# Performance work log

Measured on AMD Instinct MI355X. Metric: run time of the kernel, lower is better.

Reference implementation:

```python
import jax, jax.numpy as jnp
import numpy as np

N_NODES = 100000
N_EDGES = 1600000
IN_CH, HID, OUT_CH = 512, 128, 64
K_HOPS = 2
LN_EPS = 1e-5


def _layernorm(h, gamma, beta):
    mu = jnp.mean(h, axis=-1, keepdims=True)
    var = jnp.var(h, axis=-1, keepdims=True)
    return (h - mu) * jax.lax.rsqrt(var + LN_EPS) * gamma + beta


def setup_inputs() -> dict:
    key = jax.random.key(0)
    ks = jax.random.split(key, 12)
    x = jax.random.normal(ks[0], (N_NODES, IN_CH), dtype=jnp.float32)
    edge_index = jax.random.randint(ks[1], (2, N_EDGES), 0, N_NODES, dtype=jnp.int64)
    s1 = 1.0 / np.sqrt(IN_CH)
    s2 = 1.0 / np.sqrt(HID)
    return {
        "x": x,
        "edge_index": edge_index,
        "W1": jax.random.normal(ks[2], (IN_CH, HID), dtype=jnp.float32) * s1,
        "b1": jnp.zeros((HID,), dtype=jnp.float32),
        "g1": jnp.ones((HID,), dtype=jnp.float32),
        "be1": jnp.zeros((HID,), dtype=jnp.float32),
        "Wc": jax.random.normal(ks[3], (HID, HID), dtype=jnp.float32) * s2,
        "bc": jnp.zeros((HID,), dtype=jnp.float32),
        "g2": jnp.ones((HID,), dtype=jnp.float32),
        "be2": jnp.zeros((HID,), dtype=jnp.float32),
        "W2": jax.random.normal(ks[4], (HID, OUT_CH), dtype=jnp.float32) * s2,
        "b2": jnp.zeros((OUT_CH,), dtype=jnp.float32),
    }


def reference(x, edge_index, W1, b1, g1, be1, Wc, bc, g2, be2, W2, b2):
    N = x.shape[0]
    # lin1 -> GELU(exact) -> LayerNorm (dropout is identity in eval)
    h = jax.nn.gelu(x @ W1 + b1, approximate=False)
    h = _layernorm(h, g1, be1)

    # SGConv: add self-loops, symmetric normalization, K-hop propagation, then Linear
    loop = jnp.arange(N, dtype=edge_index.dtype)
    src = jnp.concatenate([edge_index[0], loop])
    dst = jnp.concatenate([edge_index[1], loop])
    w = jnp.ones(src.shape[0], dtype=h.dtype)
    deg = jax.ops.segment_sum(w, dst, num_segments=N)
    dinv = jnp.where(deg > 0, jax.lax.rsqrt(deg), 0.0)
    norm = (dinv[src] * dinv[dst])[:, None]  # [E+N, 1]
    for _ in range(K_HOPS):
        h = jax.ops.segment_sum(h[src] * norm, dst, num_segments=N)
    h = h @ Wc + bc

    h = jax.nn.gelu(h, approximate=False)
    h = _layernorm(h, g2, be2)
    return h @ W2 + b2
```

## Files before the change

kernel.cpp:

```cpp
#include <hip/hip_runtime.h>
#include <math.h>

#define N_NODES 100000
#define N_EDGES 1600000
#define IN_CH 512
#define HID 128
#define OUT_CH 64
#define NBUCK ((N_NODES + 255) / 256)
#define LBUF_CAP 8192

typedef __attribute__((ext_vector_type(8))) short bf16x8;
typedef __attribute__((ext_vector_type(4))) float f32x4;

__device__ __forceinline__ float gelu_exact(float v) {
    return 0.5f * v * (1.0f + erff(v * 0.70710678118654752440f));
}

__device__ __forceinline__ unsigned short bf16r(float f) {
    union { float f; unsigned int u; } v;
    v.f = f;
    unsigned int r = v.u + 0x7fffu + ((v.u >> 16) & 1u);
    return (unsigned short)(r >> 16);
}

__device__ __forceinline__ float bf16f(unsigned short h) {
    union { unsigned int u; float f; } v;
    v.u = ((unsigned int)h) << 16;
    return v.f;
}

__global__ void bzero(int* __restrict__ bcnt) {
    if (threadIdx.x < NBUCK) bcnt[threadIdx.x] = 0;
}

__global__ __launch_bounds__(256) void bhist(const int* __restrict__ dst,
                                             int* __restrict__ bcnt, int e) {
    __shared__ int lcnt[NBUCK];
    for (int i = threadIdx.x; i < NBUCK; i += 256) lcnt[i] = 0;
    __syncthreads();
    int base = blockIdx.x * 256 * 16 + threadIdx.x;
#pragma unroll
    for (int i = 0; i < 16; i++) {
        int id = base + i * 256;
        if (id < e) atomicAdd(&lcnt[dst[id] >> 8], 1);
    }
    __syncthreads();
    for (int i = threadIdx.x; i < NBUCK; i += 256)
        if (lcnt[i]) atomicAdd(&bcnt[i], lcnt[i]);
}

__global__ void bscan(const int* __restrict__ bcnt, int* __restrict__ bbase,
                      int* __restrict__ bcur, int* __restrict__ rowptr, int e) {
    __shared__ int tmp[512];
    int i = threadIdx.x;
    int v = (i < NBUCK) ? bcnt[i] : 0;
    tmp[i] = v;
    __syncthreads();
#pragma unroll
    for (int o = 1; o < 512; o <<= 1) {
        int t = (i >= o) ? tmp[i - o] : 0;
        __syncthreads();
        tmp[i] += t;
        __syncthreads();
    }
    if (i <= NBUCK) {
        int excl = (i == 0) ? 0 : tmp[i - 1];
        bbase[i] = excl;
        if (i < NBUCK) bcur[i] = excl;
    }
    if (i == 0) rowptr[N_NODES] = e;
}

__global__ __launch_bounds__(256) void binA(const int* __restrict__ src,
                                            const int* __restrict__ dst,
                                            int* __restrict__ bcur,
                                            unsigned int* __restrict__ ebuf, int e) {
    __shared__ int lcnt[NBUCK];
    __shared__ int gbase[NBUCK];
    const int tid = threadIdx.x;
    for (int i = tid; i < NBUCK; i += 256) lcnt[i] = 0;
    __syncthreads();
    const int base = blockIdx.x * (256 * 16);
    int sv[16];
    short bk[16], rk[16];
    unsigned char ld[16];
#pragma unroll
    for (int i = 0; i < 16; i++) {
        int idx = base + tid + i * 256;
        bk[i] = -1;
        if (idx < e) {
            int d = dst[idx];
            sv[i] = src[idx];
            ld[i] = (unsigned char)(d & 255);
            int b = d >> 8;
            bk[i] = (short)b;
            rk[i] = (short)atomicAdd(&lcnt[b], 1);
        }
    }
    __syncthreads();
    for (int i = tid; i < NBUCK; i += 256)
        if (lcnt[i]) gbase[i] = atomicAdd(&bcur[i], lcnt[i]);
    __syncthreads();
#pragma unroll
    for (int i = 0; i < 16; i++)
        if (bk[i] >= 0)
            ebuf[gbase[bk[i]] + rk[i]] = ((unsigned int)sv[i] << 8) | ld[i];
}

__global__ __launch_bounds__(256) void binB(const unsigned int* __restrict__ ebuf,
                                            const int* __restrict__ bbase,
                                            int* __restrict__ rowptr, int* __restrict__ eadj,
                                            float* __restrict__ dinv) {
    __shared__ int cnt[256], lofs[256], lcur[256];
    __shared__ int lbuf[LBUF_CAP];
    const int b = blockIdx.x, tid = threadIdx.x;
    const int n0 = b * 256;
    const int nn = min(256, N_NODES - n0);
    const int e0 = bbase[b], e1 = bbase[b + 1];
    const int ecount = e1 - e0;
    cnt[tid] = 0;
    __syncthreads();
    for (int i = tid; i < ecount; i += 256) atomicAdd(&cnt[ebuf[e0 + i] & 255], 1);
    __syncthreads();
    int v = cnt[tid];
    lofs[tid] = v;
    __syncthreads();
#pragma unroll
    for (int o = 1; o < 256; o <<= 1) {
        int t = (tid >= o) ? lofs[tid - o] : 0;
        __syncthreads();
        lofs[tid] += t;
        __syncthreads();
    }
    int excl = lofs[tid] - v;
    lcur[tid] = excl;
    if (tid < nn) {
        rowptr[n0 + tid] = e0 + excl;
        dinv[n0 + tid] = rsqrtf((float)(v + 1));
    }
    __syncthreads();
    for (int i = tid; i < ecount; i += 256) {
        unsigned int w = ebuf[e0 + i];
        int pos = atomicAdd(&lcur[w & 255], 1);
        int s = (int)(w >> 8);
        if (pos < LBUF_CAP) lbuf[pos] = s;
        else eadj[e0 + pos] = s;
    }
    __syncthreads();
    int lim = min(ecount, LBUF_CAP);
    for (int i = tid; i < lim; i += 256) eadj[e0 + i] = lbuf[i];
}

__global__ void conv_t(const float* __restrict__ in, unsigned short* __restrict__ out,
                       int Kdim, int Nc) {
    int idx = blockIdx.x * 256 + threadIdx.x;
    if (idx >= Kdim * Nc) return;
    int n = idx / Kdim, k = idx % Kdim;
    out[idx] = bf16r(in[(size_t)k * Nc + n]);
}

template <int K, int NT, bool A32, bool LN>
__global__ __launch_bounds__(256) void gemm_mfma(
    const void* __restrict__ Aptr, const unsigned short* __restrict__ BT,
    const float* __restrict__ bias, const float* __restrict__ gamma,
    const float* __restrict__ beta, void* __restrict__ Cptr, int M) {
    constexpr int BM = 64, N = NT * 16, NSTEP = K / 32;
    __shared__ unsigned short As[2][BM * 32];
    __shared__ unsigned short Bs[2][N * 32];
    const int tid = threadIdx.x;
    const int wave = tid >> 6, lane = tid & 63;
    const int l15 = lane & 15, quad = lane >> 4;
    const int row0 = blockIdx.x * BM;

    const int sr = tid >> 2, sc = tid & 3;
    const int sswz = sc ^ ((sr >> 2) & 3);
    const bool aok = (row0 + sr) < M;

    const float* A32p = (const float*)Aptr + (size_t)(row0 + sr) * K + sc * 8;
    const unsigned short* A16p = (const unsigned short*)Aptr + (size_t)(row0 + sr) * K + sc * 8;
    const unsigned short* B0p = BT + (size_t)sr * K + sc * 8;
    const unsigned short* B1p = BT + (size_t)(sr + 64) * K + sc * 8;

    float4 pa0, pa1;
    int4 pa16, pb0, pb1;
    if (A32) {
        pa0 = aok ? *(const float4*)(A32p) : make_float4(0.f, 0.f, 0.f, 0.f);
        pa1 = aok ? *(const float4*)(A32p + 4) : make_float4(0.f, 0.f, 0.f, 0.f);
    } else {
        pa16 = aok ? *(const int4*)(A16p) : make_int4(0, 0, 0, 0);
    }
    pb0 = *(const int4*)(B0p);
    if (NT == 8) pb1 = *(const int4*)(B1p);

    f32x4 acc[NT];
#pragma unroll
    for (int ni = 0; ni < NT; ni++) acc[ni] = (f32x4){0.f, 0.f, 0.f, 0.f};

    float bia[NT], gam[NT], bet[NT];
#pragma unroll
    for (int ni = 0; ni < NT; ni++) {
        bia[ni] = bias[ni * 16 + l15];
        if (LN) {
            gam[ni] = gamma[ni * 16 + l15];
            bet[ni] = beta[ni * 16 + l15];
        }
    }

    const int fswz = quad ^ ((l15 >> 2) & 3);
    const int aoff = (wave * 16 + l15) * 32 + fswz * 8;

    for (int step = 0; step < NSTEP; step++) {
        const int buf = step & 1;
        if (A32) {
            int4 w;
            w.x = (int)((unsigned int)bf16r(pa0.x) | ((unsigned int)bf16r(pa0.y) << 16));
            w.y = (int)((unsigned int)bf16r(pa0.z) | ((unsigned int)bf16r(pa0.w) << 16));
            w.z = (int)((unsigned int)bf16r(pa1.x) | ((unsigned int)bf16r(pa1.y) << 16));
            w.w = (int)((unsigned int)bf16r(pa1.z) | ((unsigned int)bf16r(pa1.w) << 16));
            *(int4*)&As[buf][sr * 32 + sswz * 8] = w;
        } else {
            *(int4*)&As[buf][sr * 32 + sswz * 8] = pa16;
        }
        *(int4*)&Bs[buf][sr * 32 + sswz * 8] = pb0;
        if (NT == 8) *(int4*)&Bs[buf][(sr + 64) * 32 + sswz * 8] = pb1;
        __syncthreads();
        if (step + 1 < NSTEP) {
            const int ko = (step + 1) * 32;
            if (A32) {
                pa0 = aok ? *(const float4*)(A32p + ko) : make_float4(0.f, 0.f, 0.f, 0.f);
                pa1 = aok ? *(const float4*)(A32p + ko + 4) : make_float4(0.f, 0.f, 0.f, 0.f);
            } else {
                pa16 = aok ? *(const int4*)(A16p + ko) : make_int4(0, 0, 0, 0);
            }
            pb0 = *(const int4*)(B0p + ko);
            if (NT == 8) pb1 = *(const int4*)(B1p + ko);
        }
        bf16x8 a = *(const bf16x8*)&As[buf][aoff];
#pragma unroll
        for (int ni = 0; ni < NT; ni++) {
            bf16x8 b = *(const bf16x8*)&Bs[buf][(ni * 16 + l15) * 32 + fswz * 8];
            acc[ni] = __builtin_amdgcn_mfma_f32_16x16x32_bf16(a, b, acc[ni], 0, 0, 0);
        }
    }

#pragma unroll
    for (int r = 0; r < 4; r++) {
        int grow = row0 + wave * 16 + quad * 4 + r;
        if (LN) {
            float g[NT];
            float s = 0.f, sq = 0.f;
#pragma unroll
            for (int ni = 0; ni < NT; ni++) {
                float v = gelu_exact(acc[ni][r] + bia[ni]);
                g[ni] = v;
                s += v;
                sq += v * v;
            }
#pragma unroll
            for (int m = 1; m < 16; m <<= 1) {
                s += __shfl_xor(s, m);
                sq += __shfl_xor(sq, m);
            }
            float mu = s * (1.0f / N);
            float var = sq * (1.0f / N) - mu * mu;
            float rs = rsqrtf(var + 1e-5f);
            if (grow < M) {
                unsigned short* C = (unsigned short*)Cptr;
#pragma unroll
                for (int ni = 0; ni < NT; ni++) {
                    float o = (g[ni] - mu) * rs * gam[ni] + bet[ni];
                    C[(size_t)grow * N + ni * 16 + l15] = bf16r(o);
                }
            }
        } else {
            if (grow < M) {
                float* C = (float*)Cptr;
#pragma unroll
                for (int ni = 0; ni < NT; ni++)
                    C[(size_t)grow * N + ni * 16 + l15] = acc[ni][r] + bia[ni];
            }
        }
    }
}

__global__ __launch_bounds__(256) void sgc_gather_bf16(const unsigned short* __restrict__ hin,
                                                       unsigned short* __restrict__ hout,
                                                       const int* __restrict__ rowptr,
                                                       const int* __restrict__ eadj,
                                                       const float* __restrict__ dinv, int n) {
    int row = blockIdx.x * 4 + (threadIdx.x >> 6);
    int lane = threadIdx.x & 63;
    if (row >= n) return;
    float di = dinv[row];
    unsigned int u = *(const unsigned int*)(hin + (size_t)row * HID + lane * 2);
    float ax = bf16f((unsigned short)(u & 0xffff)) * di * di;
    float ay = bf16f((unsigned short)(u >> 16)) * di * di;
    int j = rowptr[row], end = rowptr[row + 1];
    for (; j + 7 < end; j += 8) {
        int s[8];
        float dv[8];
        unsigned int uu[8];
#pragma unroll
        for (int t = 0; t < 8; t++) s[t] = eadj[j + t];
#pragma unroll
        for (int t = 0; t < 8; t++) dv[t] = dinv[s[t]];
#pragma unroll
        for (int t = 0; t < 8; t++)
            uu[t] = *(const unsigned int*)(hin + (size_t)s[t] * HID + lane * 2);
#pragma unroll
        for (int t = 0; t < 8; t++) {
            float w = di * dv[t];
            ax += bf16f((unsigned short)(uu[t] & 0xffff)) * w;
            ay += bf16f((unsigned short)(uu[t] >> 16)) * w;
        }
    }
    for (; j + 1 < end; j += 2) {
        int s0 = eadj[j], s1 = eadj[j + 1];
        float w0 = di * dinv[s0], w1 = di * dinv[s1];
        unsigned int u0 = *(const unsigned int*)(hin + (size_t)s0 * HID + lane * 2);
        unsigned int u1 = *(const unsigned int*)(hin + (size_t)s1 * HID + lane * 2);
        ax += bf16f((unsigned short)(u0 & 0xffff)) * w0 + bf16f((unsigned short)(u1 & 0xffff)) * w1;
        ay += bf16f((unsigned short)(u0 >> 16)) * w0 + bf16f((unsigned short)(u1 >> 16)) * w1;
    }
    if (j < end) {
        int s0 = eadj[j];
        float w = di * dinv[s0];
        unsigned int u0 = *(const unsigned int*)(hin + (size_t)s0 * HID + lane * 2);
        ax += bf16f((unsigned short)(u0 & 0xffff)) * w;
        ay += bf16f((unsigned short)(u0 >> 16)) * w;
    }
    unsigned int o = (unsigned int)bf16r(ax) | ((unsigned int)bf16r(ay) << 16);
    *(unsigned int*)(hout + (size_t)row * HID + lane * 2) = o;
}

extern "C" void kernel_launch(void* const* d_in, const int* in_sizes, int n_in,
                              void* d_out, int out_size, void* d_ws, size_t ws_size,
                              hipStream_t stream) {
    const float* x   = (const float*)d_in[0];
    const int*   ei  = (const int*)d_in[1];
    const float* W1  = (const float*)d_in[2];
    const float* b1  = (const float*)d_in[3];
    const float* g1  = (const float*)d_in[4];
    const float* be1 = (const float*)d_in[5];
    const float* Wc  = (const float*)d_in[6];
    const float* bc  = (const float*)d_in[7];
    const float* g2  = (const float*)d_in[8];
    const float* be2 = (const float*)d_in[9];
    const float* W2  = (const float*)d_in[10];
    const float* b2  = (const float*)d_in[11];
    float* out = (float*)d_out;

    const int N = in_sizes[0] / IN_CH;
    const int E = in_sizes[1] / 2;
    const int* src = ei;
    const int* dst = ei + E;

    char* ws = (char*)d_ws;
    size_t off = 0;
    auto alloc = [&](size_t bytes) {
        void* p = ws + off;
        off = (off + bytes + 255) & ~(size_t)255;
        return p;
    };
    float* dinv   = (float*)alloc((size_t)N * 4);
    int*   rowptr = (int*)alloc((size_t)(N + 1) * 4);
    int*   bcnt   = (int*)alloc((size_t)(NBUCK + 1) * 4);
    int*   bbase  = (int*)alloc((size_t)(NBUCK + 1) * 4);
    int*   bcur   = (int*)alloc((size_t)(NBUCK + 1) * 4);
    unsigned int* ebuf = (unsigned int*)alloc((size_t)E * 4);
    int*   eadj   = (int*)alloc((size_t)E * 4);
    unsigned short* W1T = (unsigned short*)alloc((size_t)HID * IN_CH * 2);
    unsigned short* WcT = (unsigned short*)alloc((size_t)HID * HID * 2);
    unsigned short* W2T = (unsigned short*)alloc((size_t)OUT_CH * HID * 2);
    unsigned short* hA  = (unsigned short*)alloc((size_t)N * HID * 2);
    unsigned short* hB  = (unsigned short*)alloc((size_t)N * HID * 2);

    const int B = 256;
    const int eblk16 = (E + 4095) / 4096;

    bzero<<<1, 512, 0, stream>>>(bcnt);
    bhist<<<eblk16, B, 0, stream>>>(dst, bcnt, E);
    bscan<<<1, 512, 0, stream>>>(bcnt, bbase, bcur, rowptr, E);
    binA<<<eblk16, B, 0, stream>>>(src, dst, bcur, ebuf, E);
    binB<<<NBUCK, B, 0, stream>>>(ebuf, bbase, rowptr, eadj, dinv);

    conv_t<<<(IN_CH * HID + 255) / 256, B, 0, stream>>>(W1, W1T, IN_CH, HID);
    conv_t<<<(HID * HID + 255) / 256, B, 0, stream>>>(Wc, WcT, HID, HID);
    conv_t<<<(HID * OUT_CH + 255) / 256, B, 0, stream>>>(W2, W2T, HID, OUT_CH);

    const int gblk = (N + 63) / 64;
    gemm_mfma<IN_CH, 8, true, true><<<gblk, B, 0, stream>>>(x, W1T, b1, g1, be1, hA, N);
    sgc_gather_bf16<<<(N + 3) / 4, B, 0, stream>>>(hA, hB, rowptr, eadj, dinv, N);
    sgc_gather_bf16<<<(N + 3) / 4, B, 0, stream>>>(hB, hA, rowptr, eadj, dinv, N);
    gemm_mfma<HID, 8, false, true><<<gblk, B, 0, stream>>>(hA, WcT, bc, g2, be2, hB, N);
    gemm_mfma<HID, 4, false, false><<<gblk, B, 0, stream>>>(hB, W2T, b2, nullptr, nullptr, out, N);
}
```

Baseline: 539.4 us.

## Fold symmetric normalization into node pre/post scaling and simplify gather

After: 530.2 us. About the same (-1.7%).

```diff
diff --git a/kernel.cpp b/kernel.cpp
--- a/kernel.cpp
+++ b/kernel.cpp
@@ -151,19 +151,37 @@
     for (int i = tid; i < lim; i += 256) eadj[e0 + i] = lbuf[i];
 }
 
-__global__ void conv_t(const float* __restrict__ in, unsigned short* __restrict__ out,
-                       int Kdim, int Nc) {
+__global__ __launch_bounds__(256) void conv_all(const float* __restrict__ W1,
+                                                const float* __restrict__ Wc,
+                                                const float* __restrict__ W2,
+                                                unsigned short* __restrict__ W1T,
+                                                unsigned short* __restrict__ WcT,
+                                                unsigned short* __restrict__ W2T) {
     int idx = blockIdx.x * 256 + threadIdx.x;
-    if (idx >= Kdim * Nc) return;
-    int n = idx / Kdim, k = idx % Kdim;
-    out[idx] = bf16r(in[(size_t)k * Nc + n]);
-}
-
-template <int K, int NT, bool A32, bool LN>
+    if (idx < IN_CH * HID) {
+        int n = idx / IN_CH, k = idx % IN_CH;
+        W1T[idx] = bf16r(W1[(size_t)k * HID + n]);
+        return;
+    }
+    idx -= IN_CH * HID;
+    if (idx < HID * HID) {
+        int n = idx / HID, k = idx % HID;
+        WcT[idx] = bf16r(Wc[(size_t)k * HID + n]);
+        return;
+    }
+    idx -= HID * HID;
+    if (idx < HID * OUT_CH) {
+        int n = idx / HID, k = idx % HID;
+        W2T[idx] = bf16r(W2[(size_t)k * OUT_CH + n]);
+    }
+}
+
+template <int K, int NT, bool A32, bool LN, bool SCALE>
 __global__ __launch_bounds__(256) void gemm_mfma(
     const void* __restrict__ Aptr, const unsigned short* __restrict__ BT,
     const float* __restrict__ bias, const float* __restrict__ gamma,
-    const float* __restrict__ beta, void* __restrict__ Cptr, int M) {
+    const float* __restrict__ beta, const float* __restrict__ dinvp,
+    void* __restrict__ Cptr, int M) {
     constexpr int BM = 64, N = NT * 16, NSTEP = K / 32;
     __shared__ unsigned short As[2][BM * 32];
     __shared__ unsigned short Bs[2][N * 32];
@@ -265,10 +283,13 @@
             float var = sq * (1.0f / N) - mu * mu;
             float rs = rsqrtf(var + 1e-5f);
             if (grow < M) {
+                float dv = 1.0f;
+                if (SCALE) dv = dinvp[grow];
                 unsigned short* C = (unsigned short*)Cptr;
 #pragma unroll
                 for (int ni = 0; ni < NT; ni++) {
                     float o = (g[ni] - mu) * rs * gam[ni] + bet[ni];
+                    if (SCALE) o *= dv;
                     C[(size_t)grow * N + ni * 16 + l15] = bf16r(o);
                 }
             }
@@ -287,48 +308,40 @@
                                                        unsigned short* __restrict__ hout,
                                                        const int* __restrict__ rowptr,
                                                        const int* __restrict__ eadj,
-                                                       const float* __restrict__ dinv, int n) {
-    int row = blockIdx.x * 4 + (threadIdx.x >> 6);
-    int lane = threadIdx.x & 63;
+                                                       const float* __restrict__ dinv,
+                                                       int n, int pw) {
+    int row = __builtin_amdgcn_readfirstlane(blockIdx.x * 4 + (threadIdx.x >> 6));
     if (row >= n) return;
-    float di = dinv[row];
-    unsigned int u = *(const unsigned int*)(hin + (size_t)row * HID + lane * 2);
-    float ax = bf16f((unsigned short)(u & 0xffff)) * di * di;
-    float ay = bf16f((unsigned short)(u >> 16)) * di * di;
-    int j = rowptr[row], end = rowptr[row + 1];
+    const int lane = threadIdx.x & 63;
+    const unsigned int* __restrict__ rows = (const unsigned int*)hin;
+    unsigned int u = rows[(size_t)row * 64 + lane];
+    float ax = bf16f((unsigned short)(u & 0xffff));
+    float ay = bf16f((unsigned short)(u >> 16));
+    int j = rowptr[row];
+    const int end = rowptr[row + 1];
     for (; j + 7 < end; j += 8) {
         int s[8];
-        float dv[8];
+#pragma unroll
+        for (int t = 0; t < 8; t++) s[t] = __builtin_amdgcn_readfirstlane(eadj[j + t]);
         unsigned int uu[8];
 #pragma unroll
-        for (int t = 0; t < 8; t++) s[t] = eadj[j + t];
-#pragma unroll
-        for (int t = 0; t < 8; t++) dv[t] = dinv[s[t]];
-#pragma unroll
-        for (int t = 0; t < 8; t++)
-            uu[t] = *(const unsigned int*)(hin + (size_t)s[t] * HID + lane * 2);
+        for (int t = 0; t < 8; t++) uu[t] = rows[(size_t)s[t] * 64 + lane];
 #pragma unroll
         for (int t = 0; t < 8; t++) {
-            float w = di * dv[t];
-            ax += bf16f((unsigned short)(uu[t] & 0xffff)) * w;
-            ay += bf16f((unsigned short)(uu[t] >> 16)) * w;
-        }
-    }
-    for (; j + 1 < end; j += 2) {
-        int s0 = eadj[j], s1 = eadj[j + 1];
-        float w0 = di * dinv[s0], w1 = di * dinv[s1];
-        unsigned int u0 = *(const unsigned int*)(hin + (size_t)s0 * HID + lane * 2);
-        unsigned int u1 = *(const unsigned int*)(hin + (size_t)s1 * HID + lane * 2);
-        ax += bf16f((unsigned short)(u0 & 0xffff)) * w0 + bf16f((unsigned short)(u1 & 0xffff)) * w1;
-        ay += bf16f((unsigned short)(u0 >> 16)) * w0 + bf16f((unsigned short)(u1 >> 16)) * w1;
-    }
-    if (j < end) {
-        int s0 = eadj[j];
-        float w = di * dinv[s0];
-        unsigned int u0 = *(const unsigned int*)(hin + (size_t)s0 * HID + lane * 2);
-        ax += bf16f((unsigned short)(u0 & 0xffff)) * w;
-        ay += bf16f((unsigned short)(u0 >> 16)) * w;
-    }
+            ax += bf16f((unsigned short)(uu[t] & 0xffff));
+            ay += bf16f((unsigned short)(uu[t] >> 16));
+        }
+    }
+    for (; j < end; j++) {
+        int s0 = __builtin_amdgcn_readfirstlane(eadj[j]);
+        unsigned int u0 = rows[(size_t)s0 * 64 + lane];
+        ax += bf16f((unsigned short)(u0 & 0xffff));
+        ay += bf16f((unsigned short)(u0 >> 16));
+    }
+    float di = dinv[row];
+    float sc = (pw == 2) ? di * di : di;
+    ax *= sc;
+    ay *= sc;
     unsigned int o = (unsigned int)bf16r(ax) | ((unsigned int)bf16r(ay) << 16);
     *(unsigned int*)(hout + (size_t)row * HID + lane * 2) = o;
 }
@@ -384,14 +397,13 @@
     binA<<<eblk16, B, 0, stream>>>(src, dst, bcur, ebuf, E);
     binB<<<NBUCK, B, 0, stream>>>(ebuf, bbase, rowptr, eadj, dinv);
 
-    conv_t<<<(IN_CH * HID + 255) / 256, B, 0, stream>>>(W1, W1T, IN_CH, HID);
-    conv_t<<<(HID * HID + 255) / 256, B, 0, stream>>>(Wc, WcT, HID, HID);
-    conv_t<<<(HID * OUT_CH + 255) / 256, B, 0, stream>>>(W2, W2T, HID, OUT_CH);
+    const int convtot = IN_CH * HID + HID * HID + HID * OUT_CH;
+    conv_all<<<(convtot + 255) / 256, B, 0, stream>>>(W1, Wc, W2, W1T, WcT, W2T);
 
     const int gblk = (N + 63) / 64;
-    gemm_mfma<IN_CH, 8, true, true><<<gblk, B, 0, stream>>>(x, W1T, b1, g1, be1, hA, N);
-    sgc_gather_bf16<<<(N + 3) / 4, B, 0, stream>>>(hA, hB, rowptr, eadj, dinv, N);
-    sgc_gather_bf16<<<(N + 3) / 4, B, 0, stream>>>(hB, hA, rowptr, eadj, dinv, N);
-    gemm_mfma<HID, 8, false, true><<<gblk, B, 0, stream>>>(hA, WcT, bc, g2, be2, hB, N);
-    gemm_mfma<HID, 4, false, false><<<gblk, B, 0, stream>>>(hB, W2T, b2, nullptr, nullptr, out, N);
-}
+    gemm_mfma<IN_CH, 8, true, true, true><<<gblk, B, 0, stream>>>(x, W1T, b1, g1, be1, dinv, hA, N);
+    sgc_gather_bf16<<<(N + 3) / 4, B, 0, stream>>>(hA, hB, rowptr, eadj, dinv, N, 2);
+    sgc_gather_bf16<<<(N + 3) / 4, B, 0, stream>>>(hB, hA, rowptr, eadj, dinv, N, 1);
+    gemm_mfma<HID, 8, false, true, false><<<gblk, B, 0, stream>>>(hA, WcT, bc, g2, be2, nullptr, hB, N);
+    gemm_mfma<HID, 4, false, false, false><<<gblk, B, 0, stream>>>(hB, W2T, b2, nullptr, nullptr, nullptr, out, N);
+}
```
